# Kernel optimization log

Hardware: AMD Instinct MI355X
Metric: run time of the kernel (lower is better)

## Reference

```python
import jax, jax.numpy as jnp
import numpy as np

B, G, P, E, H, K = 16, 512, 512, 256, 16, 16
CLIP = 10.0

def setup_inputs() -> dict:
    key = jax.random.key(0)
    ks = jax.random.split(key, 10)
    d = {
        "input1": jax.random.normal(ks[0], (B, 1, E), jnp.float32),
        "input2": jax.random.normal(ks[1], (B, G, E), jnp.float32),
        "current_time": jax.random.uniform(ks[2], (B, G, 1), jnp.float32),
        "ninf_mask": jnp.zeros((B, G, P), jnp.float32),
        "encoded_nodes": jax.random.normal(ks[3], (B, P, E), jnp.float32),
        # learned params (Linear weights stored [in, out]; y = x @ W)
        "Wq": jax.random.normal(ks[4], (2 * E + 1, H * K), jnp.float32) / np.sqrt(2 * E + 1),
        "Wk": jax.random.normal(ks[5], (E, H * K), jnp.float32) / np.sqrt(E),
        "Wv": jax.random.normal(ks[6], (E, H * K), jnp.float32) / np.sqrt(E),
        "Wc_w": jax.random.normal(ks[7], (H * K, E), jnp.float32) / np.sqrt(H * K),
        "Wc_b": jax.random.normal(ks[8], (E,), jnp.float32) * 0.01,
    }
    return d

def _heads(x):  # [B, N, H*K] -> [B, H, N, K]
    b, n, _ = x.shape
    return x.reshape(b, n, H, K).transpose(0, 2, 1, 3)

def reference(input1, input2, current_time, ninf_mask, encoded_nodes, Wq, Wk, Wv, Wc_w, Wc_b):
    # reset(): precompute k, v, single_head_key from encoded_nodes
    k = _heads(encoded_nodes @ Wk)  # [B,H,P,K]
    v = _heads(encoded_nodes @ Wv)  # [B,H,P,K]

    # forward()
    input_cat = jnp.concatenate(
        (jnp.broadcast_to(input1, (B, G, E)), input2, current_time), axis=2)  # [B,G,2E+1]
    q = _heads(input_cat @ Wq)  # [B,H,G,K]

    # MHA with additive ninf mask
    score = jnp.einsum("bhgk,bhpk->bhgp", q, k) / np.sqrt(K)
    score = score + ninf_mask[:, None, :, :]
    weights = jax.nn.softmax(score, axis=3)
    out = jnp.einsum("bhgp,bhpk->bhgk", weights, v)
    out_concat = out.transpose(0, 2, 1, 3).reshape(B, G, H * K)
    mh_atten_out = out_concat @ Wc_w + Wc_b  # [B,G,E]

    # single-head pointer score with tanh clipping
    score2 = jnp.einsum("bge,bpe->bgp", mh_atten_out, encoded_nodes) / np.sqrt(E)
    score_clipped = CLIP * jnp.tanh(score2)
    probs = jax.nn.softmax(score_clipped + ninf_mask, axis=2)
    return probs
```

## Files before the change

### kernel.cpp

```cpp
#include <hip/hip_runtime.h>
#include <math.h>

#define BB 16
#define GG 512
#define PP 512
#define EE 256
#define HH 16
#define KD 16
#define HK 256

typedef __bf16 bf16x8 __attribute__((ext_vector_type(8)));
typedef __bf16 bf16x4 __attribute__((ext_vector_type(4)));
typedef float f32x4 __attribute__((ext_vector_type(4)));
typedef float f32x16 __attribute__((ext_vector_type(16)));

#define SA_STRIDE 40
#define SMEM_BYTES 30720

__device__ inline void cvt_split8(const float* __restrict__ p, bf16x8& h, bf16x8& l)
{
    float4 f0 = *(const float4*)p;
    float4 f1 = *(const float4*)(p + 4);
    float v[8] = {f0.x, f0.y, f0.z, f0.w, f1.x, f1.y, f1.z, f1.w};
#pragma unroll
    for (int j = 0; j < 8; ++j) {
        __bf16 hh = (__bf16)v[j];
        h[j] = hh;
        l[j] = (__bf16)(v[j] - (float)hh);
    }
}

__global__ __launch_bounds__(256) void weight_prep(const float* __restrict__ Wk,
                                                   const float* __restrict__ Wv,
                                                   const float* __restrict__ Wq,
                                                   const float* __restrict__ Wc,
                                                   __bf16* __restrict__ wkt_h, __bf16* __restrict__ wkt_l,
                                                   __bf16* __restrict__ wvt_h, __bf16* __restrict__ wvt_l,
                                                   __bf16* __restrict__ wqt_h, __bf16* __restrict__ wqt_l,
                                                   __bf16* __restrict__ wct_h, __bf16* __restrict__ wct_l)
{
    int id = blockIdx.x * 256 + threadIdx.x;
    const float* W;
    __bf16 *th, *tl;
    int kbits;
    if (id < 65536)       { W = Wk; th = wkt_h; tl = wkt_l; kbits = 8; }
    else if (id < 131072) { id -= 65536;  W = Wv; th = wvt_h; tl = wvt_l; kbits = 8; }
    else if (id < 262144) { id -= 131072; W = Wq; th = wqt_h; tl = wqt_l; kbits = 9; }
    else                  { id -= 262144; W = Wc; th = wct_h; tl = wct_l; kbits = 8; }
    const int Kd = 1 << kbits;
    const int k = id & (Kd - 1);
    const int n = id >> kbits;
    const float v = W[(size_t)k * HK + n];
    const __bf16 h = (__bf16)v;
    th[((size_t)n << kbits) + k] = h;
    tl[((size_t)n << kbits) + k] = (__bf16)(v - (float)h);
}

__device__ inline void kvproj_body(int bx, int tid, unsigned char* smem,
                                   const float* __restrict__ A,
                                   const __bf16* __restrict__ Bkh,
                                   const __bf16* __restrict__ Bkl,
                                   const __bf16* __restrict__ Bvh,
                                   const __bf16* __restrict__ Bvl,
                                   __bf16* __restrict__ Khi,
                                   __bf16* __restrict__ Klo,
                                   __bf16* __restrict__ Vt)
{
    __bf16* sAh = (__bf16*)smem;
    __bf16* sAl = sAh + 64 * SA_STRIDE;
    __bf16* sB  = sAl + 64 * SA_STRIDE;

    const int lane = tid & 63;
    const int w = __builtin_amdgcn_readfirstlane(tid >> 6);
    const int m0 = (bx >> 2) * 64;
    const int n0 = (bx & 3) * 64;
    const int wm = (w >> 1) * 32, wn = (w & 1) * 32;
    const int ln = lane & 15, kq = (lane >> 4) * 8;
    const int ar = tid >> 2, ac = (tid & 3) * 8;

    const __bf16* bsel = (w == 0) ? Bkh : (w == 1) ? Bkl : (w == 2) ? Bvh : Bvl;

    f32x4 ak[2][2], av[2][2];
#pragma unroll
    for (int i = 0; i < 2; ++i)
#pragma unroll
        for (int j = 0; j < 2; ++j) {
            ak[i][j] = (f32x4){0.f, 0.f, 0.f, 0.f};
            av[i][j] = (f32x4){0.f, 0.f, 0.f, 0.f};
        }

    for (int k0 = 0; k0 < EE; k0 += 32) {
        {
            bf16x8 h8, l8;
            cvt_split8(A + (size_t)(m0 + ar) * EE + k0 + ac, h8, l8);
            *(bf16x8*)&sAh[ar * SA_STRIDE + ac] = h8;
            *(bf16x8*)&sAl[ar * SA_STRIDE + ac] = l8;
        }
        {
            const __bf16* src = bsel + (size_t)(n0 + lane) * EE + k0;
            __bf16* dst = sB + (w * 64 + lane) * SA_STRIDE;
            *(bf16x8*)&dst[0]  = *(const bf16x8*)&src[0];
            *(bf16x8*)&dst[8]  = *(const bf16x8*)&src[8];
            *(bf16x8*)&dst[16] = *(const bf16x8*)&src[16];
            *(bf16x8*)&dst[24] = *(const bf16x8*)&src[24];
        }
        __syncthreads();

        bf16x8 ah[2], al[2];
#pragma unroll
        for (int mt = 0; mt < 2; ++mt) {
            ah[mt] = *(const bf16x8*)&sAh[(wm + mt * 16 + ln) * SA_STRIDE + kq];
            al[mt] = *(const bf16x8*)&sAl[(wm + mt * 16 + ln) * SA_STRIDE + kq];
        }
#pragma unroll
        for (int nt = 0; nt < 2; ++nt) {
            const int rowb = wn + nt * 16 + ln;
            bf16x8 bkh8 = *(const bf16x8*)&sB[(0 * 64 + rowb) * SA_STRIDE + kq];
            bf16x8 bkl8 = *(const bf16x8*)&sB[(1 * 64 + rowb) * SA_STRIDE + kq];
            bf16x8 bvh8 = *(const bf16x8*)&sB[(2 * 64 + rowb) * SA_STRIDE + kq];
            bf16x8 bvl8 = *(const bf16x8*)&sB[(3 * 64 + rowb) * SA_STRIDE + kq];
#pragma unroll
            for (int mt = 0; mt < 2; ++mt) {
                ak[mt][nt] = __builtin_amdgcn_mfma_f32_16x16x32_bf16(ah[mt], bkh8, ak[mt][nt], 0, 0, 0);
                ak[mt][nt] = __builtin_amdgcn_mfma_f32_16x16x32_bf16(al[mt], bkh8, ak[mt][nt], 0, 0, 0);
                ak[mt][nt] = __builtin_amdgcn_mfma_f32_16x16x32_bf16(ah[mt], bkl8, ak[mt][nt], 0, 0, 0);
                av[mt][nt] = __builtin_amdgcn_mfma_f32_16x16x32_bf16(ah[mt], bvh8, av[mt][nt], 0, 0, 0);
                av[mt][nt] = __builtin_amdgcn_mfma_f32_16x16x32_bf16(al[mt], bvh8, av[mt][nt], 0, 0, 0);
                av[mt][nt] = __builtin_amdgcn_mfma_f32_16x16x32_bf16(ah[mt], bvl8, av[mt][nt], 0, 0, 0);
            }
        }
        __syncthreads();
    }

    __bf16* eKh = (__bf16*)smem;
    __bf16* eKl = eKh + 5120;
    __bf16* eV  = eKl + 5120;

    const int rbase = (lane >> 4) * 4;
#pragma unroll
    for (int mt = 0; mt < 2; ++mt)
#pragma unroll
        for (int nt = 0; nt < 2; ++nt) {
            const int hloc = (w & 1) * 2 + nt;
            const int nl = wn + nt * 16 + ln;
#pragma unroll
            for (int r = 0; r < 4; ++r) {
                const int m = wm + mt * 16 + rbase + r;
                const float vk = ak[mt][nt][r];
                const __bf16 hk = (__bf16)vk;
                eKh[(hloc * 64 + m) * 20 + ln] = hk;
                eKl[(hloc * 64 + m) * 20 + ln] = (__bf16)(vk - (float)hk);
                eV[nl * 68 + m] = (__bf16)av[mt][nt][r];
            }
        }
    __syncthreads();

    const int b = m0 >> 9;
    const int pbase = m0 & (PP - 1);
    {
        const int hl = tid >> 6, p = tid & 63;
        const int hg = (n0 >> 4) + hl;
        const size_t dst = (((size_t)b * HH + hg) * PP + pbase + p) * KD;
        const int base = (hl * 64 + p) * 20;
        uint2 a0 = *(const uint2*)&eKh[base + 0];
        uint2 a1 = *(const uint2*)&eKh[base + 4];
        uint2 a2 = *(const uint2*)&eKh[base + 8];
        uint2 a3 = *(const uint2*)&eKh[base + 12];
        *(uint4*)(Khi + dst)     = make_uint4(a0.x, a0.y, a1.x, a1.y);
        *(uint4*)(Khi + dst + 8) = make_uint4(a2.x, a2.y, a3.x, a3.y);
        uint2 c0 = *(const uint2*)&eKl[base + 0];
        uint2 c1 = *(const uint2*)&eKl[base + 4];
        uint2 c2 = *(const uint2*)&eKl[base + 8];
        uint2 c3 = *(const uint2*)&eKl[base + 12];
        *(uint4*)(Klo + dst)     = make_uint4(c0.x, c0.y, c1.x, c1.y);
        *(uint4*)(Klo + dst + 8) = make_uint4(c2.x, c2.y, c3.x, c3.y);
    }
    {
        const int n = tid >> 2, qq = tid & 3;
        const int ng = n0 + n, hg = ng >> 4, kk = ng & 15;
        const int base = n * 68 + qq * 16;
        uint2 v0 = *(const uint2*)&eV[base + 0];
        uint2 v1 = *(const uint2*)&eV[base + 4];
        uint2 v2 = *(const uint2*)&eV[base + 8];
        uint2 v3 = *(const uint2*)&eV[base + 12];
        const size_t dst = ((((size_t)b * HH + hg) * KD + kk) * PP) + pbase + qq * 16;
        *(uint4*)(Vt + dst)     = make_uint4(v0.x, v0.y, v1.x, v1.y);
        *(uint4*)(Vt + dst + 8) = make_uint4(v2.x, v2.y, v3.x, v3.y);
    }
}

__device__ inline void qproj_body(int bx, int tid, unsigned char* smem,
                                  const float* __restrict__ in1,
                                  const float* __restrict__ in2,
                                  const float* __restrict__ ct,
                                  const __bf16* __restrict__ Bh,
                                  const __bf16* __restrict__ Bl,
                                  const float* __restrict__ WqFull,
                                  __bf16* __restrict__ Qhi,
                                  __bf16* __restrict__ Qlo)
{
    __bf16* sAh = (__bf16*)smem;
    __bf16* sAl = sAh + 64 * SA_STRIDE;
    __bf16* sB  = sAl + 64 * SA_STRIDE;

    const int lane = tid & 63;
    const int w = __builtin_amdgcn_readfirstlane(tid >> 6);
    const int m0 = (bx >> 2) * 64;
    const int n0 = (bx & 3) * 64;
    const int wm = (w >> 1) * 32, wn = (w & 1) * 32;
    const int ln = lane & 15, kq = (lane >> 4) * 8;
    const int ar = tid >> 2, ac = (tid & 3) * 8;
    const int b = m0 >> 9;
    const float* WqLast = WqFull + (size_t)512 * HK;

    f32x4 acc[2][2];
#pragma unroll
    for (int i = 0; i < 2; ++i)
#pragma unroll
        for (int j = 0; j < 2; ++j) acc[i][j] = (f32x4){0.f, 0.f, 0.f, 0.f};

    for (int k0 = 0; k0 < 512; k0 += 32) {
        {
            const float* ap = (k0 < 256)
                ? in1 + (size_t)b * EE + k0 + ac
                : in2 + (size_t)(m0 + ar) * EE + (k0 - 256) + ac;
            bf16x8 h8, l8;
            cvt_split8(ap, h8, l8);
            *(bf16x8*)&sAh[ar * SA_STRIDE + ac] = h8;
            *(bf16x8*)&sAl[ar * SA_STRIDE + ac] = l8;
        }
        {
            const int mat = w >> 1;
            const int row = (w & 1) * 32 + (lane >> 1);
            const int half = (lane & 1) * 16;
            const __bf16* src = (mat ? Bl : Bh) + ((size_t)(n0 + row) << 9) + k0 + half;
            __bf16* dst = sB + (mat * 64 + row) * SA_STRIDE + half;
            *(bf16x8*)&dst[0] = *(const bf16x8*)&src[0];
            *(bf16x8*)&dst[8] = *(const bf16x8*)&src[8];
        }
        __syncthreads();

        bf16x8 ah[2], al[2];
#pragma unroll
        for (int mt = 0; mt < 2; ++mt) {
            ah[mt] = *(const bf16x8*)&sAh[(wm + mt * 16 + ln) * SA_STRIDE + kq];
            al[mt] = *(const bf16x8*)&sAl[(wm + mt * 16 + ln) * SA_STRIDE + kq];
        }
#pragma unroll
        for (int nt = 0; nt < 2; ++nt) {
            const int rowb = wn + nt * 16 + ln;
            bf16x8 bh8 = *(const bf16x8*)&sB[(0 * 64 + rowb) * SA_STRIDE + kq];
            bf16x8 bl8 = *(const bf16x8*)&sB[(1 * 64 + rowb) * SA_STRIDE + kq];
#pragma unroll
            for (int mt = 0; mt < 2; ++mt) {
                acc[mt][nt] = __builtin_amdgcn_mfma_f32_16x16x32_bf16(ah[mt], bh8, acc[mt][nt], 0, 0, 0);
                acc[mt][nt] = __builtin_amdgcn_mfma_f32_16x16x32_bf16(al[mt], bh8, acc[mt][nt], 0, 0, 0);
                acc[mt][nt] = __builtin_amdgcn_mfma_f32_16x16x32_bf16(ah[mt], bl8, acc[mt][nt], 0, 0, 0);
            }
        }
        __syncthreads();
    }

    __bf16* eQh = (__bf16*)smem;
    __bf16* eQl = eQh + 5120;

    const int rbase = (lane >> 4) * 4;
#pragma unroll
    for (int mt = 0; mt < 2; ++mt)
#pragma unroll
        for (int nt = 0; nt < 2; ++nt) {
            const int hloc = (w & 1) * 2 + nt;
            const int ng = n0 + wn + nt * 16 + ln;
            const float wq = WqLast[ng];
#pragma unroll
            for (int r = 0; r < 4; ++r) {
                const int m = wm + mt * 16 + rbase + r;
                const float v = acc[mt][nt][r] + ct[m0 + m] * wq;
                const __bf16 h = (__bf16)v;
                eQh[(hloc * 64 + m) * 20 + ln] = h;
                eQl[(hloc * 64 + m) * 20 + ln] = (__bf16)(v - (float)h);
            }
        }
    __syncthreads();

    {
        const int hl = tid >> 6, p = tid & 63;
        const int hg = (n0 >> 4) + hl;
        const int g = (m0 & (GG - 1)) + p;
        const size_t dst = (((size_t)b * HH + hg) * GG + g) * KD;
        const int base = (hl * 64 + p) * 20;
        uint2 a0 = *(const uint2*)&eQh[base + 0];
        uint2 a1 = *(const uint2*)&eQh[base + 4];
        uint2 a2 = *(const uint2*)&eQh[base + 8];
        uint2 a3 = *(const uint2*)&eQh[base + 12];
        *(uint4*)(Qhi + dst)     = make_uint4(a0.x, a0.y, a1.x, a1.y);
        *(uint4*)(Qhi + dst + 8) = make_uint4(a2.x, a2.y, a3.x, a3.y);
        uint2 c0 = *(const uint2*)&eQl[base + 0];
        uint2 c1 = *(const uint2*)&eQl[base + 4];
        uint2 c2 = *(const uint2*)&eQl[base + 8];
        uint2 c3 = *(const uint2*)&eQl[base + 12];
        *(uint4*)(Qlo + dst)     = make_uint4(c0.x, c0.y, c1.x, c1.y);
        *(uint4*)(Qlo + dst + 8) = make_uint4(c2.x, c2.y, c3.x, c3.y);
    }
}

__global__ __launch_bounds__(256, 2) void fused_proj(const float* __restrict__ enc,
                                                     const __bf16* __restrict__ Bkh,
                                                     const __bf16* __restrict__ Bkl,
                                                     const __bf16* __restrict__ Bvh,
                                                     const __bf16* __restrict__ Bvl,
                                                     __bf16* __restrict__ Khi,
                                                     __bf16* __restrict__ Klo,
                                                     __bf16* __restrict__ Vt,
                                                     const float* __restrict__ in1,
                                                     const float* __restrict__ in2,
                                                     const float* __restrict__ ct,
                                                     const __bf16* __restrict__ Bqh,
                                                     const __bf16* __restrict__ Bql,
                                                     const float* __restrict__ WqFull,
                                                     __bf16* __restrict__ Qhi,
                                                     __bf16* __restrict__ Qlo)
{
    __shared__ __align__(16) unsigned char smem[SMEM_BYTES];
    const int id = blockIdx.x;
    if (id < 512)
        kvproj_body(id, threadIdx.x, smem, enc, Bkh, Bkl, Bvh, Bvl, Khi, Klo, Vt);
    else
        qproj_body(id - 512, threadIdx.x, smem, in1, in2, ct, Bqh, Bql, WqFull, Qhi, Qlo);
}

__global__ __launch_bounds__(256, 4) void attn_v8(const __bf16* __restrict__ Qhi,
                                                  const __bf16* __restrict__ Qlo,
                                                  const __bf16* __restrict__ Khi,
                                                  const __bf16* __restrict__ Klo,
                                                  const __bf16* __restrict__ Vt,
                                                  const float* __restrict__ mask,
                                                  __bf16* __restrict__ Ath,
                                                  __bf16* __restrict__ Atl)
{
    __shared__ __align__(16) __bf16 sP[4][32][40];
    __shared__ float srs[4][32];

    const int t = threadIdx.x;
    const int lane = t & 63;
    const int w = __builtin_amdgcn_readfirstlane(t >> 6);
    const int g0 = blockIdx.x * 32;
    const int h = blockIdx.y * 4 + w;
    const int b = blockIdx.z;
    const int ln32 = lane & 31;
    const int half = lane >> 5;
    const int ln16 = lane & 15;
    const int quad = (lane >> 4) & 3;

    const size_t qbase = (((size_t)b * HH + h) * GG + g0) * KD;
    const size_t kbase = ((size_t)b * HH + h) * PP * KD;
    const size_t vbase = ((size_t)b * HH + h) * KD * PP;
    const float* mbase = mask + ((size_t)(b * GG + g0)) * PP;

    bf16x8 qah = *(const bf16x8*)(Qhi + qbase + (size_t)ln32 * KD + half * 8);
    bf16x8 qal = *(const bf16x8*)(Qlo + qbase + (size_t)ln32 * KD + half * 8);

    float rs[16];
#pragma unroll
    for (int r = 0; r < 16; ++r) rs[r] = 0.f;
    f32x4 o0 = (f32x4){0.f, 0.f, 0.f, 0.f};
    f32x4 o1 = (f32x4){0.f, 0.f, 0.f, 0.f};

#pragma unroll 2
    for (int pc = 0; pc < 16; ++pc) {
        const int pb = pc * 32;
        const size_t ko = kbase + (size_t)(pb + ln32) * KD + half * 8;
        bf16x8 kh = *(const bf16x8*)(Khi + ko);
        bf16x8 kl = *(const bf16x8*)(Klo + ko);

        f32x16 s = (f32x16){0.f, 0.f, 0.f, 0.f, 0.f, 0.f, 0.f, 0.f,
                            0.f, 0.f, 0.f, 0.f, 0.f, 0.f, 0.f, 0.f};
        s = __builtin_amdgcn_mfma_f32_32x32x16_bf16(qah, kh, s, 0, 0, 0);
        s = __builtin_amdgcn_mfma_f32_32x32x16_bf16(qal, kh, s, 0, 0, 0);
        s = __builtin_amdgcn_mfma_f32_32x32x16_bf16(qah, kl, s, 0, 0, 0);

#pragma unroll
        for (int r = 0; r < 16; ++r) {
            const int row = (r & 3) + 8 * (r >> 2) + 4 * half;
            const float m = mbase[(size_t)row * PP + pb + ln32];
            const float e = __expf(s[r] * 0.25f + m);
            rs[r] += e;
            sP[w][row][ln32] = (__bf16)e;
        }

        bf16x8 vb = *(const bf16x8*)(Vt + vbase + (size_t)ln16 * PP + pb + quad * 8);
        bf16x8 p0 = *(const bf16x8*)&sP[w][ln16][quad * 8];
        bf16x8 p1 = *(const bf16x8*)&sP[w][16 + ln16][quad * 8];
        o0 = __builtin_amdgcn_mfma_f32_16x16x32_bf16(p0, vb, o0, 0, 0, 0);
        o1 = __builtin_amdgcn_mfma_f32_16x16x32_bf16(p1, vb, o1, 0, 0, 0);
    }

#pragma unroll
    for (int r = 0; r < 16; ++r) {
#pragma unroll
        for (int mm = 1; mm < 32; mm <<= 1) rs[r] += __shfl_xor(rs[r], mm);
    }
    if (ln32 == 0) {
#pragma unroll
        for (int r = 0; r < 16; ++r)
            srs[w][(r & 3) + 8 * (r >> 2) + 4 * half] = rs[r];
    }

#pragma unroll
    for (int t2 = 0; t2 < 2; ++t2) {
        const f32x4 oc = t2 ? o1 : o0;
#pragma unroll
        for (int r = 0; r < 4; ++r) {
            const int grow = t2 * 16 + quad * 4 + r;
            const float v = oc[r] / srs[w][grow];
            const __bf16 hv = (__bf16)v;
            const size_t oo = ((size_t)(b * GG + g0 + grow)) * HK + h * KD + ln16;
            Ath[oo] = hv;
            Atl[oo] = (__bf16)(v - (float)hv);
        }
    }
}

__device__ inline void outproj_body(int bx, int tid,
                                    const __bf16* __restrict__ Ah,
                                    const __bf16* __restrict__ Al,
                                    const __bf16* __restrict__ Bh,
                                    const __bf16* __restrict__ Bl,
                                    const float* __restrict__ bias,
                                    __bf16* __restrict__ Ch,
                                    __bf16* __restrict__ Cl)
{
    const int lane = tid & 63, w = tid >> 6;
    const int m0 = (bx >> 2) * 64 + (w >> 1) * 32;
    const int n0 = (bx & 3) * 64 + (w & 1) * 32;
    const int ln = lane & 15, kc = (lane >> 4) * 8;

    f32x4 acc[2][2];
#pragma unroll
    for (int i = 0; i < 2; ++i)
#pragma unroll
        for (int j = 0; j < 2; ++j) acc[i][j] = (f32x4){0.f, 0.f, 0.f, 0.f};

    for (int k0 = 0; k0 < EE; k0 += 32) {
        bf16x8 ah[2], al[2], bh[2], bl[2];
#pragma unroll
        for (int mt = 0; mt < 2; ++mt) {
            const size_t o = (size_t)(m0 + mt * 16 + ln) * EE + k0 + kc;
            ah[mt] = *(const bf16x8*)(Ah + o);
            al[mt] = *(const bf16x8*)(Al + o);
        }
#pragma unroll
        for (int nt = 0; nt < 2; ++nt) {
            const size_t o = (size_t)(n0 + nt * 16 + ln) * EE + k0 + kc;
            bh[nt] = *(const bf16x8*)(Bh + o);
            bl[nt] = *(const bf16x8*)(Bl + o);
        }
#pragma unroll
        for (int mt = 0; mt < 2; ++mt)
#pragma unroll
            for (int nt = 0; nt < 2; ++nt) {
                acc[mt][nt] = __builtin_amdgcn_mfma_f32_16x16x32_bf16(ah[mt], bh[nt], acc[mt][nt], 0, 0, 0);
                acc[mt][nt] = __builtin_amdgcn_mfma_f32_16x16x32_bf16(al[mt], bh[nt], acc[mt][nt], 0, 0, 0);
                acc[mt][nt] = __builtin_amdgcn_mfma_f32_16x16x32_bf16(ah[mt], bl[nt], acc[mt][nt], 0, 0, 0);
            }
    }

    const int rbase = (lane >> 4) * 4;
#pragma unroll
    for (int mt = 0; mt < 2; ++mt)
#pragma unroll
        for (int nt = 0; nt < 2; ++nt)
#pragma unroll
            for (int r = 0; r < 4; ++r) {
                const int m = m0 + rbase + r + mt * 16;
                const int n = n0 + nt * 16 + ln;
                const float v = acc[mt][nt][r] + bias[n];
                const __bf16 h = (__bf16)v;
                Ch[(size_t)m * HK + n] = h;
                Cl[(size_t)m * HK + n] = (__bf16)(v - (float)h);
            }
}

__global__ __launch_bounds__(256) void fused_post(const __bf16* __restrict__ Ah,
                                                  const __bf16* __restrict__ Al,
                                                  const __bf16* __restrict__ Bh,
                                                  const __bf16* __restrict__ Bl,
                                                  const float* __restrict__ bias,
                                                  __bf16* __restrict__ Ch,
                                                  __bf16* __restrict__ Cl,
                                                  const float* __restrict__ enc,
                                                  __bf16* __restrict__ enc_h,
                                                  __bf16* __restrict__ enc_l)
{
    const int id = blockIdx.x;
    if (id < 512) {
        outproj_body(id, threadIdx.x, Ah, Al, Bh, Bl, bias, Ch, Cl);
    } else {
        const int i = ((id - 512) * 256 + threadIdx.x) * 4;
        float4 v = *(const float4*)(enc + i);
        bf16x4 h, l;
        h[0] = (__bf16)v.x; l[0] = (__bf16)(v.x - (float)h[0]);
        h[1] = (__bf16)v.y; l[1] = (__bf16)(v.y - (float)h[1]);
        h[2] = (__bf16)v.z; l[2] = (__bf16)(v.z - (float)h[2]);
        h[3] = (__bf16)v.w; l[3] = (__bf16)(v.w - (float)h[3]);
        *(bf16x4*)(enc_h + i) = h;
        *(bf16x4*)(enc_l + i) = l;
    }
}

__global__ __launch_bounds__(512) void pointer_v3(const __bf16* __restrict__ mh_hi,
                                                  const __bf16* __restrict__ mh_lo,
                                                  const __bf16* __restrict__ enc_hi,
                                                  const __bf16* __restrict__ enc_lo,
                                                  const float* __restrict__ mask,
                                                  float* __restrict__ out)
{
    __shared__ float swsum[8][32];
    const int t = threadIdx.x;
    const int lane = t & 63;
    const int w = __builtin_amdgcn_readfirstlane(t >> 6);
    const int id = blockIdx.x;
    const int b = id & 15;
    const int g0 = (id >> 4) * 32;
    const int ln32 = lane & 31;
    const int half = lane >> 5;

    const size_t arow = ((size_t)(b * GG + g0 + ln32)) * EE + half * 8;
    const size_t brow = ((size_t)(b * PP + w * 64 + ln32)) * EE + half * 8;

    f32x16 acc[2];
#pragma unroll
    for (int pt = 0; pt < 2; ++pt)
        acc[pt] = (f32x16){0.f, 0.f, 0.f, 0.f, 0.f, 0.f, 0.f, 0.f,
                           0.f, 0.f, 0.f, 0.f, 0.f, 0.f, 0.f, 0.f};

    for (int kc = 0; kc < EE; kc += 16) {
        bf16x8 ah = *(const bf16x8*)(mh_hi + arow + kc);
        bf16x8 al = *(const bf16x8*)(mh_lo + arow + kc);
#pragma unroll
        for (int pt = 0; pt < 2; ++pt) {
            const size_t bo = brow + (size_t)pt * 32 * EE + kc;
            bf16x8 bh = *(const bf16x8*)(enc_hi + bo);
            bf16x8 bl = *(const bf16x8*)(enc_lo + bo);
            acc[pt] = __builtin_amdgcn_mfma_f32_32x32x16_bf16(ah, bh, acc[pt], 0, 0, 0);
            acc[pt] = __builtin_amdgcn_mfma_f32_32x32x16_bf16(al, bh, acc[pt], 0, 0, 0);
            acc[pt] = __builtin_amdgcn_mfma_f32_32x32x16_bf16(ah, bl, acc[pt], 0, 0, 0);
        }
    }

    float rsum[16];
#pragma unroll
    for (int r = 0; r < 16; ++r) rsum[r] = 0.f;
#pragma unroll
    for (int pt = 0; pt < 2; ++pt)
#pragma unroll
        for (int r = 0; r < 16; ++r) {
            const int row = (r & 3) + 8 * (r >> 2) + 4 * half;
            float s = acc[pt][r] * 0.0625f;
            s = fminf(9.f, fmaxf(-9.f, s));
            const float e2 = __expf(2.f * s);
            const float th = (e2 - 1.f) / (e2 + 1.f);
            const float m = mask[((size_t)(b * GG + g0 + row)) * PP + w * 64 + pt * 32 + ln32];
            const float e = __expf(10.f * th + m);
            acc[pt][r] = e;
            rsum[r] += e;
        }

#pragma unroll
    for (int r = 0; r < 16; ++r) {
        rsum[r] += __shfl_xor(rsum[r], 1);
        rsum[r] += __shfl_xor(rsum[r], 2);
        rsum[r] += __shfl_xor(rsum[r], 4);
        rsum[r] += __shfl_xor(rsum[r], 8);
        rsum[r] += __shfl_xor(rsum[r], 16);
    }
    if (ln32 == 0) {
#pragma unroll
        for (int r = 0; r < 16; ++r)
            swsum[w][(r & 3) + 8 * (r >> 2) + 4 * half] = rsum[r];
    }
    __syncthreads();

    float inv[16];
#pragma unroll
    for (int r = 0; r < 16; ++r) {
        const int row = (r & 3) + 8 * (r >> 2) + 4 * half;
        float tot = 0.f;
#pragma unroll
        for (int wv = 0; wv < 8; ++wv) tot += swsum[wv][row];
        inv[r] = 1.f / tot;
    }

#pragma unroll
    for (int pt = 0; pt < 2; ++pt)
#pragma unroll
        for (int r = 0; r < 16; ++r) {
            const int row = (r & 3) + 8 * (r >> 2) + 4 * half;
            out[((size_t)(b * GG + g0 + row)) * PP + w * 64 + pt * 32 + ln32] =
                acc[pt][r] * inv[r];
        }
}

extern "C" void kernel_launch(void* const* d_in, const int* in_sizes, int n_in,
                              void* d_out, int out_size, void* d_ws, size_t ws_size,
                              hipStream_t stream)
{
    const float* in1  = (const float*)d_in[0];
    const float* in2  = (const float*)d_in[1];
    const float* ct   = (const float*)d_in[2];
    const float* mask = (const float*)d_in[3];
    const float* enc  = (const float*)d_in[4];
    const float* Wq   = (const float*)d_in[5];
    const float* Wk   = (const float*)d_in[6];
    const float* Wv   = (const float*)d_in[7];
    const float* Wcw  = (const float*)d_in[8];
    const float* Wcb  = (const float*)d_in[9];
    float* out = (float*)d_out;
    float* ws  = (float*)d_ws;

    const size_t SEG = (size_t)BB * GG * HK;
    __bf16* Khi = (__bf16*)ws;
    __bf16* Klo = Khi + SEG;
    __bf16* Vt  = (__bf16*)(ws + SEG);
    __bf16* Ath = Vt + SEG;
    __bf16* Qhi = (__bf16*)(ws + 2 * SEG);
    __bf16* Qlo = Qhi + SEG;
    __bf16* wkt_h = (__bf16*)(ws + 3 * SEG);
    __bf16* wkt_l = wkt_h + 65536;
    __bf16* wvt_h = wkt_l + 65536;
    __bf16* wvt_l = wvt_h + 65536;
    __bf16* wqt_h = wvt_l + 65536;
    __bf16* wqt_l = wqt_h + 131072;
    __bf16* wct_h = wqt_l + 131072;
    __bf16* wct_l = wct_h + 65536;
    __bf16* Atl   = (__bf16*)(ws + 3 * SEG) + 1048576;
    __bf16* mh_h  = (__bf16*)ws;
    __bf16* mh_l  = mh_h + SEG;
    __bf16* enc_h = (__bf16*)(ws + 2 * SEG);
    __bf16* enc_l = enc_h + SEG;

    const dim3 blk(256);

    weight_prep<<<dim3(1280), blk, 0, stream>>>(Wk, Wv, Wq, Wcw,
                                                wkt_h, wkt_l, wvt_h, wvt_l,
                                                wqt_h, wqt_l, wct_h, wct_l);

    fused_proj<<<dim3(1024), blk, 0, stream>>>(enc, wkt_h, wkt_l, wvt_h, wvt_l,
                                               Khi, Klo, Vt,
                                               in1, in2, ct, wqt_h, wqt_l, Wq,
                                               Qhi, Qlo);

    attn_v8<<<dim3(GG / 32, HH / 4, BB), blk, 0, stream>>>(Qhi, Qlo, Khi, Klo, Vt, mask, Ath, Atl);

    fused_post<<<dim3(2560), blk, 0, stream>>>(Ath, Atl, wct_h, wct_l, Wcb,
                                               mh_h, mh_l, enc, enc_h, enc_l);

    pointer_v3<<<dim3(256), dim3(512), 0, stream>>>(mh_h, mh_l, enc_h, enc_l, mask, out);
}
```

Baseline: 204.0 us.

## Factor broadcast input1 term out of Q projection and pre-split inputs to bf16

The input1 part of the Q projection is the same for every row in a batch, so it is now computed once per batch as a small fp32 vector (q1) in a prep kernel and added in the Q epilogue. This halves the K-loop of the Q GEMM. The prep kernel also pre-splits encoded_nodes and input2 into bf16 hi/lo once, replacing the per-tile conversion inside the projection GEMMs. The enc split moves out of fused_post, and fused_proj's occupancy hint goes from 2 to 3. The cost is extra workspace traffic for the split copies and a naive scalar loop for q1.

```diff
diff --git a/kernel.cpp b/kernel.cpp
--- a/kernel.cpp
+++ b/kernel.cpp
@@ -17,47 +17,67 @@
 #define SA_STRIDE 40
 #define SMEM_BYTES 30720
 
-__device__ inline void cvt_split8(const float* __restrict__ p, bf16x8& h, bf16x8& l)
-{
-    float4 f0 = *(const float4*)p;
-    float4 f1 = *(const float4*)(p + 4);
-    float v[8] = {f0.x, f0.y, f0.z, f0.w, f1.x, f1.y, f1.z, f1.w};
-#pragma unroll
-    for (int j = 0; j < 8; ++j) {
-        __bf16 hh = (__bf16)v[j];
-        h[j] = hh;
-        l[j] = (__bf16)(v[j] - (float)hh);
-    }
-}
-
-__global__ __launch_bounds__(256) void weight_prep(const float* __restrict__ Wk,
-                                                   const float* __restrict__ Wv,
-                                                   const float* __restrict__ Wq,
-                                                   const float* __restrict__ Wc,
-                                                   __bf16* __restrict__ wkt_h, __bf16* __restrict__ wkt_l,
-                                                   __bf16* __restrict__ wvt_h, __bf16* __restrict__ wvt_l,
-                                                   __bf16* __restrict__ wqt_h, __bf16* __restrict__ wqt_l,
-                                                   __bf16* __restrict__ wct_h, __bf16* __restrict__ wct_l)
-{
-    int id = blockIdx.x * 256 + threadIdx.x;
-    const float* W;
-    __bf16 *th, *tl;
-    int kbits;
-    if (id < 65536)       { W = Wk; th = wkt_h; tl = wkt_l; kbits = 8; }
-    else if (id < 131072) { id -= 65536;  W = Wv; th = wvt_h; tl = wvt_l; kbits = 8; }
-    else if (id < 262144) { id -= 131072; W = Wq; th = wqt_h; tl = wqt_l; kbits = 9; }
-    else                  { id -= 262144; W = Wc; th = wct_h; tl = wct_l; kbits = 8; }
-    const int Kd = 1 << kbits;
-    const int k = id & (Kd - 1);
-    const int n = id >> kbits;
-    const float v = W[(size_t)k * HK + n];
-    const __bf16 h = (__bf16)v;
-    th[((size_t)n << kbits) + k] = h;
-    tl[((size_t)n << kbits) + k] = (__bf16)(v - (float)h);
+__global__ __launch_bounds__(256) void prep(const float* __restrict__ Wq,
+                                            const float* __restrict__ Wk,
+                                            const float* __restrict__ Wv,
+                                            const float* __restrict__ Wc,
+                                            const float* __restrict__ in1,
+                                            const float* __restrict__ enc,
+                                            const float* __restrict__ in2,
+                                            __bf16* __restrict__ wkt_h, __bf16* __restrict__ wkt_l,
+                                            __bf16* __restrict__ wvt_h, __bf16* __restrict__ wvt_l,
+                                            __bf16* __restrict__ wqt_h, __bf16* __restrict__ wqt_l,
+                                            __bf16* __restrict__ wct_h, __bf16* __restrict__ wct_l,
+                                            __bf16* __restrict__ enc_h, __bf16* __restrict__ enc_l,
+                                            __bf16* __restrict__ in2h, __bf16* __restrict__ in2l,
+                                            float* __restrict__ q1)
+{
+    int gid = blockIdx.x * 256 + threadIdx.x;
+    if (gid < 4096) {
+        const int b = gid >> 8, n = gid & 255;
+        const float* ip = in1 + (size_t)b * EE;
+        float acc = 0.f;
+#pragma unroll 4
+        for (int k = 0; k < EE; ++k) acc += ip[k] * Wq[(size_t)k * HK + n];
+        q1[gid] = acc;
+        return;
+    }
+    gid -= 4096;
+    if (gid < 262144) {
+        int id = gid;
+        const float* W;
+        __bf16 *th, *tl;
+        int krow = 0;
+        if (id < 65536)       { W = Wk; th = wkt_h; tl = wkt_l; }
+        else if (id < 131072) { id -= 65536;  W = Wv; th = wvt_h; tl = wvt_l; }
+        else if (id < 196608) { id -= 131072; W = Wq; th = wqt_h; tl = wqt_l; krow = 256; }
+        else                  { id -= 196608; W = Wc; th = wct_h; tl = wct_l; }
+        const int k = id & 255;
+        const int n = id >> 8;
+        const float v = W[(size_t)(k + krow) * HK + n];
+        const __bf16 h = (__bf16)v;
+        th[(n << 8) + k] = h;
+        tl[(n << 8) + k] = (__bf16)(v - (float)h);
+        return;
+    }
+    gid -= 262144;
+    const float* src;
+    __bf16 *dh, *dl;
+    if (gid < 524288) { src = enc; dh = enc_h; dl = enc_l; }
+    else              { gid -= 524288; src = in2; dh = in2h; dl = in2l; }
+    const size_t i = (size_t)gid * 4;
+    float4 v = *(const float4*)(src + i);
+    __bf16 h0 = (__bf16)v.x, h1 = (__bf16)v.y, h2 = (__bf16)v.z, h3 = (__bf16)v.w;
+    bf16x4 h = {h0, h1, h2, h3};
+    bf16x4 l = {(__bf16)(v.x - (float)h0), (__bf16)(v.y - (float)h1),
+                (__bf16)(v.z - (float)h2), (__bf16)(v.w - (float)h3)};
+    *(bf16x4*)(dh + i) = h;
+    *(bf16x4*)(dl + i) = l;
 }
 
 __device__ inline void kvproj_body(int bx, int tid, unsigned char* smem,
-                                   const float* __restrict__ A,
+                                   const __bf16* __restrict__ Ahg,
+                                   const __bf16* __restrict__ Alg,
                                    const __bf16* __restrict__ Bkh,
                                    const __bf16* __restrict__ Bkl,
                                    const __bf16* __restrict__ Bvh,
@@ -91,10 +111,9 @@
 
     for (int k0 = 0; k0 < EE; k0 += 32) {
         {
-            bf16x8 h8, l8;
-            cvt_split8(A + (size_t)(m0 + ar) * EE + k0 + ac, h8, l8);
-            *(bf16x8*)&sAh[ar * SA_STRIDE + ac] = h8;
-            *(bf16x8*)&sAl[ar * SA_STRIDE + ac] = l8;
+            const size_t ao = (size_t)(m0 + ar) * EE + k0 + ac;
+            *(bf16x8*)&sAh[ar * SA_STRIDE + ac] = *(const bf16x8*)(Ahg + ao);
+            *(bf16x8*)&sAl[ar * SA_STRIDE + ac] = *(const bf16x8*)(Alg + ao);
         }
         {
             const __bf16* src = bsel + (size_t)(n0 + lane) * EE + k0;
@@ -190,12 +209,13 @@
 }
 
 __device__ inline void qproj_body(int bx, int tid, unsigned char* smem,
-                                  const float* __restrict__ in1,
-                                  const float* __restrict__ in2,
+                                  const __bf16* __restrict__ Ahg,
+                                  const __bf16* __restrict__ Alg,
                                   const float* __restrict__ ct,
                                   const __bf16* __restrict__ Bh,
                                   const __bf16* __restrict__ Bl,
                                   const float* __restrict__ WqFull,
+                                  const float* __restrict__ q1,
                                   __bf16* __restrict__ Qhi,
                                   __bf16* __restrict__ Qlo)
 {
@@ -219,21 +239,17 @@
 #pragma unroll
         for (int j = 0; j < 2; ++j) acc[i][j] = (f32x4){0.f, 0.f, 0.f, 0.f};
 
-    for (int k0 = 0; k0 < 512; k0 += 32) {
+    for (int k0 = 0; k0 < EE; k0 += 32) {
         {
-            const float* ap = (k0 < 256)
-                ? in1 + (size_t)b * EE + k0 + ac
-                : in2 + (size_t)(m0 + ar) * EE + (k0 - 256) + ac;
-            bf16x8 h8, l8;
-            cvt_split8(ap, h8, l8);
-            *(bf16x8*)&sAh[ar * SA_STRIDE + ac] = h8;
-            *(bf16x8*)&sAl[ar * SA_STRIDE + ac] = l8;
+            const size_t ao = (size_t)(m0 + ar) * EE + k0 + ac;
+            *(bf16x8*)&sAh[ar * SA_STRIDE + ac] = *(const bf16x8*)(Ahg + ao);
+            *(bf16x8*)&sAl[ar * SA_STRIDE + ac] = *(const bf16x8*)(Alg + ao);
         }
         {
             const int mat = w >> 1;
             const int row = (w & 1) * 32 + (lane >> 1);
             const int half = (lane & 1) * 16;
-            const __bf16* src = (mat ? Bl : Bh) + ((size_t)(n0 + row) << 9) + k0 + half;
+            const __bf16* src = (mat ? Bl : Bh) + ((size_t)(n0 + row) << 8) + k0 + half;
             __bf16* dst = sB + (mat * 64 + row) * SA_STRIDE + half;
             *(bf16x8*)&dst[0] = *(const bf16x8*)&src[0];
             *(bf16x8*)&dst[8] = *(const bf16x8*)&src[8];
@@ -272,10 +288,11 @@
             const int hloc = (w & 1) * 2 + nt;
             const int ng = n0 + wn + nt * 16 + ln;
             const float wq = WqLast[ng];
+            const float q1v = q1[b * HK + ng];
 #pragma unroll
             for (int r = 0; r < 4; ++r) {
                 const int m = wm + mt * 16 + rbase + r;
-                const float v = acc[mt][nt][r] + ct[m0 + m] * wq;
+                const float v = acc[mt][nt][r] + q1v + ct[m0 + m] * wq;
                 const __bf16 h = (__bf16)v;
                 eQh[(hloc * 64 + m) * 20 + ln] = h;
                 eQl[(hloc * 64 + m) * 20 + ln] = (__bf16)(v - (float)h);
@@ -304,7 +321,8 @@
     }
 }
 
-__global__ __launch_bounds__(256, 2) void fused_proj(const float* __restrict__ enc,
+__global__ __launch_bounds__(256, 3) void fused_proj(const __bf16* __restrict__ enc_h,
+                                                     const __bf16* __restrict__ enc_l,
                                                      const __bf16* __restrict__ Bkh,
                                                      const __bf16* __restrict__ Bkl,
                                                      const __bf16* __restrict__ Bvh,
@@ -312,21 +330,22 @@
                                                      __bf16* __restrict__ Khi,
                                                      __bf16* __restrict__ Klo,
                                                      __bf16* __restrict__ Vt,
-                                                     const float* __restrict__ in1,
-                                                     const float* __restrict__ in2,
+                                                     const __bf16* __restrict__ in2h,
+                                                     const __bf16* __restrict__ in2l,
                                                      const float* __restrict__ ct,
                                                      const __bf16* __restrict__ Bqh,
                                                      const __bf16* __restrict__ Bql,
                                                      const float* __restrict__ WqFull,
+                                                     const float* __restrict__ q1,
                                                      __bf16* __restrict__ Qhi,
                                                      __bf16* __restrict__ Qlo)
 {
     __shared__ __align__(16) unsigned char smem[SMEM_BYTES];
     const int id = blockIdx.x;
     if (id < 512)
-        kvproj_body(id, threadIdx.x, smem, enc, Bkh, Bkl, Bvh, Bvl, Khi, Klo, Vt);
+        kvproj_body(id, threadIdx.x, smem, enc_h, enc_l, Bkh, Bkl, Bvh, Bvl, Khi, Klo, Vt);
     else
-        qproj_body(id - 512, threadIdx.x, smem, in1, in2, ct, Bqh, Bql, WqFull, Qhi, Qlo);
+        qproj_body(id - 512, threadIdx.x, smem, in2h, in2l, ct, Bqh, Bql, WqFull, q1, Qhi, Qlo);
 }
 
 __global__ __launch_bounds__(256, 4) void attn_v8(const __bf16* __restrict__ Qhi,
@@ -421,15 +440,16 @@
     }
 }
 
-__device__ inline void outproj_body(int bx, int tid,
-                                    const __bf16* __restrict__ Ah,
-                                    const __bf16* __restrict__ Al,
-                                    const __bf16* __restrict__ Bh,
-                                    const __bf16* __restrict__ Bl,
-                                    const float* __restrict__ bias,
-                                    __bf16* __restrict__ Ch,
-                                    __bf16* __restrict__ Cl)
-{
+__global__ __launch_bounds__(256) void fused_post(const __bf16* __restrict__ Ah,
+                                                  const __bf16* __restrict__ Al,
+                                                  const __bf16* __restrict__ Bh,
+                                                  const __bf16* __restrict__ Bl,
+                                                  const float* __restrict__ bias,
+                                                  __bf16* __restrict__ Ch,
+                                                  __bf16* __restrict__ Cl)
+{
+    const int bx = blockIdx.x;
+    const int tid = threadIdx.x;
     const int lane = tid & 63, w = tid >> 6;
     const int m0 = (bx >> 2) * 64 + (w >> 1) * 32;
     const int n0 = (bx & 3) * 64 + (w & 1) * 32;
@@ -479,33 +499,6 @@
                 Ch[(size_t)m * HK + n] = h;
                 Cl[(size_t)m * HK + n] = (__bf16)(v - (float)h);
             }
-}
-
-__global__ __launch_bounds__(256) void fused_post(const __bf16* __restrict__ Ah,
-                                                  const __bf16* __restrict__ Al,
-                                                  const __bf16* __restrict__ Bh,
-                                                  const __bf16* __restrict__ Bl,
-                                                  const float* __restrict__ bias,
-                                                  __bf16* __restrict__ Ch,
-                                                  __bf16* __restrict__ Cl,
-                                                  const float* __restrict__ enc,
-                                                  __bf16* __restrict__ enc_h,
-                                                  __bf16* __restrict__ enc_l)
-{
-    const int id = blockIdx.x;
-    if (id < 512) {
-        outproj_body(id, threadIdx.x, Ah, Al, Bh, Bl, bias, Ch, Cl);
-    } else {
-        const int i = ((id - 512) * 256 + threadIdx.x) * 4;
-        float4 v = *(const float4*)(enc + i);
-        bf16x4 h, l;
-        h[0] = (__bf16)v.x; l[0] = (__bf16)(v.x - (float)h[0]);
-        h[1] = (__bf16)v.y; l[1] = (__bf16)(v.y - (float)h[1]);
-        h[2] = (__bf16)v.z; l[2] = (__bf16)(v.z - (float)h[2]);
-        h[3] = (__bf16)v.w; l[3] = (__bf16)(v.w - (float)h[3]);
-        *(bf16x4*)(enc_h + i) = h;
-        *(bf16x4*)(enc_l + i) = l;
-    }
 }
 
 __global__ __launch_bounds__(512) void pointer_v3(const __bf16* __restrict__ mh_hi,
@@ -630,30 +623,34 @@
     __bf16* wvt_h = wkt_l + 65536;
     __bf16* wvt_l = wvt_h + 65536;
     __bf16* wqt_h = wvt_l + 65536;
-    __bf16* wqt_l = wqt_h + 131072;
-    __bf16* wct_h = wqt_l + 131072;
+    __bf16* wqt_l = wqt_h + 65536;
+    __bf16* wct_h = wqt_l + 65536;
     __bf16* wct_l = wct_h + 65536;
     __bf16* Atl   = (__bf16*)(ws + 3 * SEG) + 1048576;
     __bf16* mh_h  = (__bf16*)ws;
     __bf16* mh_l  = mh_h + SEG;
-    __bf16* enc_h = (__bf16*)(ws + 2 * SEG);
+    __bf16* enc_h = (__bf16*)(ws + 4 * SEG);
     __bf16* enc_l = enc_h + SEG;
+    __bf16* in2h  = (__bf16*)(ws + 5 * SEG);
+    __bf16* in2l  = in2h + SEG;
+    float*  q1    = ws + 6 * SEG;
 
     const dim3 blk(256);
 
-    weight_prep<<<dim3(1280), blk, 0, stream>>>(Wk, Wv, Wq, Wcw,
-                                                wkt_h, wkt_l, wvt_h, wvt_l,
-                                                wqt_h, wqt_l, wct_h, wct_l);
-
-    fused_proj<<<dim3(1024), blk, 0, stream>>>(enc, wkt_h, wkt_l, wvt_h, wvt_l,
+    prep<<<dim3(5136), blk, 0, stream>>>(Wq, Wk, Wv, Wcw, in1, enc, in2,
+                                         wkt_h, wkt_l, wvt_h, wvt_l,
+                                         wqt_h, wqt_l, wct_h, wct_l,
+                                         enc_h, enc_l, in2h, in2l, q1);
+
+    fused_proj<<<dim3(1024), blk, 0, stream>>>(enc_h, enc_l,
+                                               wkt_h, wkt_l, wvt_h, wvt_l,
                                                Khi, Klo, Vt,
-                                               in1, in2, ct, wqt_h, wqt_l, Wq,
+                                               in2h, in2l, ct, wqt_h, wqt_l, Wq, q1,
                                                Qhi, Qlo);
 
     attn_v8<<<dim3(GG / 32, HH / 4, BB), blk, 0, stream>>>(Qhi, Qlo, Khi, Klo, Vt, mask, Ath, Atl);
 
-    fused_post<<<dim3(2560), blk, 0, stream>>>(Ath, Atl, wct_h, wct_l, Wcb,
-                                               mh_h, mh_l, enc, enc_h, enc_l);
+    fused_post<<<dim3(512), blk, 0, stream>>>(Ath, Atl, wct_h, wct_l, Wcb, mh_h, mh_l);
 
     pointer_v3<<<dim3(256), dim3(512), 0, stream>>>(mh_h, mh_l, enc_h, enc_l, mask, out);
 }
```

Result: slower. 218.2 us (+6.9%).
